# Optimization experiments

Hardware: AMD Instinct MI355X
Metric: run time of the kernel (lower is better)

## Reference

```python
import jax, jax.numpy as jnp
import numpy as np

B = 64; FEAT = 16; T = 32001; BANDS = 8; ND = 16
OUT_LEN = 32000; N_TAPS = 43; K_LATE = 1024
FLIP_PROB = 0.1  # 1 - stickiness (0.9)


def _dense(k, fan_in, fan_out, scale=1.0):
    return jax.random.normal(k, (fan_in, fan_out), jnp.float32) * (scale / np.sqrt(fan_in))


def setup_inputs() -> dict:
    key = jax.random.key(0)
    ks = jax.random.split(key, 20)
    z32 = lambda n: jnp.zeros((n,), jnp.float32)
    inp = {}
    inp['x'] = jax.random.normal(ks[0], (B, FEAT), jnp.float32)
    # stand-in LSTM decoder params: (B, FEAT) -> (B, T, BANDS)
    inp['lstm_W1'] = _dense(ks[1], FEAT, 64); inp['lstm_b1'] = z32(64)
    inp['lstm_W2'] = _dense(ks[2], 64, T * BANDS); inp['lstm_b2'] = z32(T * BANDS)
    # EDCToFDNMapper params
    inp['enc_W1'] = _dense(ks[3], 2 * BANDS, 64); inp['enc_b1'] = z32(64)
    inp['enc_W2'] = _dense(ks[4], 64, 64); inp['enc_b2'] = z32(64)
    inp['del_W1'] = _dense(ks[5], 3 + 64, 64); inp['del_b1'] = z32(64)
    inp['del_W2'] = _dense(ks[6], 64, ND); inp['del_b2'] = z32(ND)
    inp['alp_W1'] = _dense(ks[7], 64, 32); inp['alp_b1'] = z32(32)
    inp['alp_W2'] = _dense(ks[8], 32, ND); inp['alp_b2'] = z32(ND)
    inp['bet_W1'] = _dense(ks[9], 64, 32); inp['bet_b1'] = z32(32)
    inp['bet_W2'] = _dense(ks[10], 32, ND); inp['bet_b2'] = z32(ND)
    # EarlyReflections gains (nn.Parameter, zeros-init in torch; random here to exercise math)
    inp['early_gains'] = jax.random.normal(ks[11], (N_TAPS,), jnp.float32) * 0.1
    # DifferentiableFDN surrogate: causal decaying FIR reverb kernel
    decay = jnp.exp(-jnp.arange(K_LATE, dtype=jnp.float32) / 256.0)
    inp['late_kernel'] = jax.random.normal(ks[12], (K_LATE,), jnp.float32) * 0.05 * decay
    # sticky-sign flip events (constant random draws, flip prob = 1 - stickiness)
    inp['flips'] = (jax.random.uniform(ks[13], (B, OUT_LEN)) < FLIP_PROB).astype(jnp.int32)
    return inp


def _causal_conv(sig, gains):
    # torch: F.conv1d(x[:,None,:], gains.flip(0)[None,None,:], padding=K-1)[:, 0, :L]
    # (torch conv1d is correlation; flipping makes it true convolution with gains)
    K = gains.shape[0]
    y = jax.lax.conv_general_dilated(sig[:, None, :], gains[::-1][None, None, :], (1,),
                                     [(K - 1, K - 1)], dimension_numbers=('NCH', 'OIH', 'NCH'))
    return y[:, 0, :sig.shape[1]]


def _mlp2(h, W1, b1, W2, b2):  # Linear-ReLU-Linear
    return jax.nn.relu(h @ W1 + b1) @ W2 + b2


def reference(x, lstm_W1, lstm_b1, lstm_W2, lstm_b2,
              enc_W1, enc_b1, enc_W2, enc_b2,
              del_W1, del_b1, del_W2, del_b2,
              alp_W1, alp_b1, alp_W2, alp_b2,
              bet_W1, bet_b1, bet_W2, bet_b2,
              early_gains, late_kernel, flips):
    Bx = x.shape[0]
    # LSTM stand-in: (B, FEAT) -> (B, T, BANDS)
    edc_pred = _mlp2(x, lstm_W1, lstm_b1, lstm_W2, lstm_b2).reshape(Bx, T, BANDS)
    edc_1d = edc_pred.mean(axis=2)  # (B, T)
    # EDCToFDNMapper
    edc_mean = edc_pred.mean(axis=1)
    q1 = edc_pred[:, :T // 4, :].mean(axis=1)
    q4 = edc_pred[:, 3 * T // 4:, :].mean(axis=1)
    edc_feat = jnp.concatenate([edc_mean, q4 - q1], axis=1)  # (B, 2*BANDS)
    h = jax.nn.relu(_mlp2(edc_feat, enc_W1, enc_b1, enc_W2, enc_b2))  # Linear-ReLU-Linear-ReLU
    delay_in = jnp.concatenate([x[:, :3], h], axis=1)
    log_kappa = _mlp2(delay_in, del_W1, del_b1, del_W2, del_b2)
    alpha_raw = _mlp2(h, alp_W1, alp_b1, alp_W2, alp_b2)
    beta_raw = _mlp2(h, bet_W1, bet_b1, bet_W2, bet_b2)
    # late reverb (FDN surrogate) + early reflections, both causal convs on edc_1d
    late = _causal_conv(edc_1d, late_kernel)[:, :OUT_LEN]   # (B, 32000)
    early = _causal_conv(edc_1d, early_gains)[:, :OUT_LEN]  # (B, 32000)
    # sign-sticky phase reconstruction: signs = (-1)^cumsum(flips[:,1:]) (parallel parity scan)
    diff = edc_1d[:, :-1] - edc_1d[:, 1:]
    amp = jnp.sqrt(jnp.clip(diff, 0.0))  # (B, T-1) == (B, 32000)
    par = jnp.cumsum(flips.at[:, 0].set(0), axis=1) % 2  # loop starts at t=1; signs[:,0]=+1
    phase = amp * (1.0 - 2.0 * par.astype(amp.dtype))
    rir = (early + late) * phase
    return (rir, edc_pred, log_kappa, alpha_raw, beta_raw)
```

## Files before the change

kernel.cpp:

```cpp
#include <hip/hip_runtime.h>
#include <hip/hip_bf16.h>

#define LJ 256008
#define TN 32001
#define OUT_LEN 32000

typedef __attribute__((ext_vector_type(8))) short short8v;
typedef __attribute__((ext_vector_type(8))) __bf16 bf16x8;
typedef __attribute__((ext_vector_type(4))) float f32x4;

__device__ __forceinline__ unsigned short f2bu(float f) {
    union { __hip_bfloat16 h; unsigned short u; } cv; cv.h = __float2bfloat16(f); return cv.u;
}
__device__ __forceinline__ uint4 pack8(const unsigned short* h) {
    return make_uint4((unsigned)h[0] | ((unsigned)h[1] << 16),
                      (unsigned)h[2] | ((unsigned)h[3] << 16),
                      (unsigned)h[4] | ((unsigned)h[5] << 16),
                      (unsigned)h[6] | ((unsigned)h[7] << 16));
}
__device__ __forceinline__ f32x4 mfma16(uint4 a, uint4 b, f32x4 c) {
    union { uint4 u; short8v s; bf16x8 v; } ua, ub;
    ua.u = a; ub.u = b;
    return __builtin_amdgcn_mfma_f32_16x16x32_bf16(ua.v, ub.v, c, 0, 0, 0);
}

__global__ __launch_bounds__(256) void k_h1(const float* __restrict__ x,
                                            const float* __restrict__ W1,
                                            const float* __restrict__ b1,
                                            float* __restrict__ h1)
{
    int idx = blockIdx.x * 256 + threadIdx.x;
    if (idx >= 4096) return;
    int b = idx >> 6, i = idx & 63;
    float acc = b1[i];
    #pragma unroll
    for (int f = 0; f < 16; ++f)
        acc += x[b * 16 + f] * W1[f * 64 + i];
    h1[i * 64 + b] = fmaxf(acc, 0.f);
}

__global__ __launch_bounds__(512) void k_gemm(const float* __restrict__ W2,
                                              const float* __restrict__ b2,
                                              const float* __restrict__ h1,
                                              float* __restrict__ edc,
                                              float* __restrict__ edc1d,
                                              float* __restrict__ P)
{
    __shared__ float h1f[4096];
    __shared__ __align__(16) unsigned short afr[4096];
    __shared__ __align__(16) unsigned short bfr[8192];
    __shared__ float wband[2048];
    __shared__ float bband[32];
    int tid = threadIdx.x;
    long C0 = (long)blockIdx.x * 256;

    #pragma unroll
    for (int s = 0; s < 8; ++s) h1f[tid + 512 * s] = h1[tid + 512 * s];
    {
        int bt = tid >> 7, kb = (tid >> 6) & 1, l = tid & 63;
        int q = l >> 4, r = l & 15;
        unsigned short hh[8];
        #pragma unroll
        for (int e = 0; e < 8; ++e)
            hh[e] = f2bu(h1[(32 * kb + 8 * q + e) * 64 + 16 * bt + r]);
        *(uint4*)(&afr[tid * 8]) = pack8(hh);
    }
    #pragma unroll
    for (int s = 0; s < 4; ++s) {
        int en = tid + 512 * s;
        int i = en >> 5, tl = en & 31;
        long c8 = C0 + 8 * tl;
        float sum = 0.f;
        if (c8 + 7 < LJ) {
            float4 u0 = *(const float4*)(W2 + (long)i * LJ + c8);
            float4 u1 = *(const float4*)(W2 + (long)i * LJ + c8 + 4);
            sum = ((u0.x + u0.y) + (u0.z + u0.w)) + ((u1.x + u1.y) + (u1.z + u1.w));
        }
        wband[i * 32 + tl] = sum;
    }
    if (tid < 32) {
        long c8 = C0 + 8 * tid;
        float sum = 0.f;
        if (c8 + 7 < LJ) {
            float4 u0 = *(const float4*)(b2 + c8);
            float4 u1 = *(const float4*)(b2 + c8 + 4);
            sum = ((u0.x + u0.y) + (u0.z + u0.w)) + ((u1.x + u1.y) + (u1.z + u1.w));
        }
        bband[tid] = sum;
    }
    #pragma unroll
    for (int s = 0; s < 2; ++s) {
        int sl = tid + 512 * s;
        int ct = sl >> 6, l = sl & 63;
        int q = l >> 4, r = l & 15;
        long col = C0 + 16 * ct + r;
        unsigned short hh[8];
        #pragma unroll
        for (int e = 0; e < 8; ++e) {
            float v = (col < LJ) ? W2[(long)(8 * q + e) * LJ + col] : 0.f;
            hh[e] = f2bu(v);
        }
        *(uint4*)(&bfr[sl * 8]) = pack8(hh);
    }
    __syncthreads();

    int lane = tid & 63, wv = tid >> 6;
    int q = lane >> 4, r = lane & 15;
    f32x4 acc[2][4];
    #pragma unroll
    for (int c = 0; c < 2; ++c)
        #pragma unroll
        for (int b = 0; b < 4; ++b) acc[c][b] = (f32x4){0.f, 0.f, 0.f, 0.f};

    #pragma unroll
    for (int ctl = 0; ctl < 2; ++ctl) {
        int ct = wv * 2 + ctl;
        uint4 braw = *(const uint4*)(&bfr[(ct * 64 + lane) * 8]);
        #pragma unroll
        for (int bt = 0; bt < 4; ++bt) {
            uint4 araw = *(const uint4*)(&afr[((bt * 2 + 0) * 64 + lane) * 8]);
            acc[ctl][bt] = mfma16(araw, braw, acc[ctl][bt]);
        }
    }
    __syncthreads();
    #pragma unroll
    for (int s = 0; s < 2; ++s) {
        int sl = tid + 512 * s;
        int ct = sl >> 6, l = sl & 63;
        int qq = l >> 4, rr = l & 15;
        long col = C0 + 16 * ct + rr;
        unsigned short hh[8];
        #pragma unroll
        for (int e = 0; e < 8; ++e) {
            float v = (col < LJ) ? W2[(long)(32 + 8 * qq + e) * LJ + col] : 0.f;
            hh[e] = f2bu(v);
        }
        *(uint4*)(&bfr[sl * 8]) = pack8(hh);
    }
    __syncthreads();
    #pragma unroll
    for (int ctl = 0; ctl < 2; ++ctl) {
        int ct = wv * 2 + ctl;
        uint4 braw = *(const uint4*)(&bfr[(ct * 64 + lane) * 8]);
        #pragma unroll
        for (int bt = 0; bt < 4; ++bt) {
            uint4 araw = *(const uint4*)(&afr[((bt * 2 + 1) * 64 + lane) * 8]);
            acc[ctl][bt] = mfma16(araw, braw, acc[ctl][bt]);
        }
    }

    #pragma unroll
    for (int s = 0; s < 4; ++s) {
        int en = tid + 512 * s;
        int b = en >> 5, tl = en & 31;
        long c8 = C0 + 8 * tl;
        if (c8 + 7 < LJ) {
            float dot = bband[tl];
            #pragma unroll 8
            for (int i = 0; i < 64; ++i)
                dot += h1f[i * 64 + b] * wband[i * 32 + tl];
            edc1d[(long)b * TN + (C0 >> 3) + tl] = dot * 0.125f;
        }
    }

    float psum[4][4];
    #pragma unroll
    for (int bt = 0; bt < 4; ++bt)
        #pragma unroll
        for (int rg = 0; rg < 4; ++rg) psum[bt][rg] = 0.f;
    #pragma unroll
    for (int ctl = 0; ctl < 2; ++ctl) {
        int ct = wv * 2 + ctl;
        long col = C0 + 16 * ct + r;
        bool okc = col < LJ;
        float bias = okc ? b2[col] : 0.f;
        #pragma unroll
        for (int bt = 0; bt < 4; ++bt) {
            #pragma unroll
            for (int rg = 0; rg < 4; ++rg) {
                float v = acc[ctl][bt][rg] + bias;
                if (okc) edc[(long)(16 * bt + 4 * q + rg) * LJ + col] = v;
                float sps = v + __shfl_xor(v, 8);
                psum[bt][rg] += sps;
            }
        }
    }
    if (r < 8) {
        #pragma unroll
        for (int bt = 0; bt < 4; ++bt)
            #pragma unroll
            for (int rg = 0; rg < 4; ++rg)
                P[(long)blockIdx.x * 512 + (16 * bt + 4 * q + rg) * 8 + r] = psum[bt][rg];
    }
}

__global__ __launch_bounds__(512) void k_redsum(const float* __restrict__ P,
                                                float* __restrict__ sums)
{
    int g = blockIdx.x, t = threadIdx.x;
    int b = t >> 3, band = t & 7;
    int s0 = g * 16, s1 = s0 + 16;
    if (s1 > 1001) s1 = 1001;
    float all = 0.f, q1 = 0.f, q4 = 0.f;
    for (int blk = s0; blk < s1; ++blk) {
        float v = P[(long)blk * 512 + t];
        all += v;
        if (blk < 250) q1 += v;
        if (blk >= 750) q4 += v;
    }
    atomicAdd(&sums[b * 24 + band * 3 + 0], all);
    atomicAdd(&sums[b * 24 + band * 3 + 1], q1);
    atomicAdd(&sums[b * 24 + band * 3 + 2], q4);
}

__global__ __launch_bounds__(64) void k_mlp(const float* __restrict__ x,
    const float* __restrict__ sums,
    const float* __restrict__ eW1, const float* __restrict__ eb1,
    const float* __restrict__ eW2, const float* __restrict__ eb2,
    const float* __restrict__ dW1, const float* __restrict__ db1,
    const float* __restrict__ dW2, const float* __restrict__ db2,
    const float* __restrict__ aW1, const float* __restrict__ ab1,
    const float* __restrict__ aW2, const float* __restrict__ ab2,
    const float* __restrict__ bW1, const float* __restrict__ bb1,
    const float* __restrict__ bW2, const float* __restrict__ bb2,
    float* __restrict__ out_lk, float* __restrict__ out_a, float* __restrict__ out_b)
{
    int b = blockIdx.x, o = threadIdx.x;
    __shared__ float feat[16], a1[64], hh[64], t1[64];
    if (o < 16) {
        float v;
        if (o < 8) v = sums[b * 24 + o * 3] * (1.f / 32001.f);
        else {
            int band = o - 8;
            v = sums[b * 24 + band * 3 + 2] * (1.f / 8001.f)
              - sums[b * 24 + band * 3 + 1] * (1.f / 8000.f);
        }
        feat[o] = v;
    }
    __syncthreads();
    {   float acc = eb1[o];
        #pragma unroll
        for (int c = 0; c < 16; ++c) acc += feat[c] * eW1[c * 64 + o];
        a1[o] = fmaxf(acc, 0.f); }
    __syncthreads();
    {   float acc = eb2[o];
        for (int c = 0; c < 64; ++c) acc += a1[c] * eW2[c * 64 + o];
        hh[o] = fmaxf(acc, 0.f); }
    __syncthreads();
    {   float acc = db1[o];
        #pragma unroll
        for (int c = 0; c < 3; ++c) acc += x[b * 16 + c] * dW1[c * 64 + o];
        for (int c = 0; c < 64; ++c) acc += hh[c] * dW1[(3 + c) * 64 + o];
        t1[o] = fmaxf(acc, 0.f); }
    __syncthreads();
    if (o < 16) {
        float acc = db2[o];
        for (int c = 0; c < 64; ++c) acc += t1[c] * dW2[c * 16 + o];
        out_lk[b * 16 + o] = acc;
    }
    __syncthreads();
    if (o < 32) {
        float acc = ab1[o];
        for (int c = 0; c < 64; ++c) acc += hh[c] * aW1[c * 32 + o];
        t1[o] = fmaxf(acc, 0.f);
    }
    __syncthreads();
    if (o < 16) {
        float acc = ab2[o];
        for (int c = 0; c < 32; ++c) acc += t1[c] * aW2[c * 16 + o];
        out_a[b * 16 + o] = acc;
    }
    __syncthreads();
    if (o < 32) {
        float acc = bb1[o];
        for (int c = 0; c < 64; ++c) acc += hh[c] * bW1[c * 32 + o];
        t1[o] = fmaxf(acc, 0.f);
    }
    __syncthreads();
    if (o < 16) {
        float acc = bb2[o];
        for (int c = 0; c < 32; ++c) acc += t1[c] * bW2[c * 16 + o];
        out_b[b * 16 + o] = acc;
    }
}

__global__ __launch_bounds__(256) void k_par1(const int* __restrict__ flips,
                                              unsigned* __restrict__ parbits,
                                              unsigned* __restrict__ ctot)
{
    int b = blockIdx.x, c = blockIdx.y, tid = threadIdx.x;
    int t = c * 256 + tid;
    int bit = (t == 0) ? 0 : (flips[(long)b * OUT_LEN + t] & 1);
    int lane = tid & 63, wv = tid >> 6;
    unsigned long long mask = __ballot(bit != 0);
    int below = ((int)__popcll(mask & ((1ull << lane) - 1ull))) & 1;
    int incl = below ^ bit;
    __shared__ int wtot[4];
    if (lane == 0) wtot[wv] = ((int)__popcll(mask)) & 1;
    __syncthreads();
    int pre = 0;
    for (int w = 0; w < wv; ++w) pre ^= wtot[w];
    int inclB = pre ^ incl;
    unsigned long long m2 = __ballot(inclB != 0);
    if (lane == 0)  parbits[b * 1000 + c * 8 + wv * 2 + 0] = (unsigned)(m2 & 0xffffffffull);
    if (lane == 32) parbits[b * 1000 + c * 8 + wv * 2 + 1] = (unsigned)(m2 >> 32);
    if (tid == 0) ctot[c * 64 + b] = (unsigned)(wtot[0] ^ wtot[1] ^ wtot[2] ^ wtot[3]);
}

__global__ __launch_bounds__(64) void k_par2(const unsigned* __restrict__ ctot,
                                             unsigned* __restrict__ cpref)
{
    int b = threadIdx.x;
    unsigned carry = 0;
    for (int c = 0; c < 125; ++c) {
        cpref[c * 64 + b] = carry;
        carry ^= ctot[c * 64 + b];
    }
}

__global__ __launch_bounds__(512) void k_convm(const float* __restrict__ edc1d,
    const float* __restrict__ lk, const float* __restrict__ eg,
    const unsigned* __restrict__ parbits, const unsigned* __restrict__ cpref,
    float* __restrict__ rir)
{
    __shared__ float kerf[1024];
    __shared__ __align__(16) unsigned short afr[33 * 64 * 8];
    __shared__ __align__(16) unsigned short sbf[3136];
    __shared__ float sf32[2049];
    int b = blockIdx.x, tb0 = blockIdx.y * 2048, tid = threadIdx.x;
    const float* src = edc1d + (long)b * TN;
    for (int k = tid; k < 1024; k += 512)
        kerf[k] = lk[k] + (k < 43 ? eg[k] : 0.f);
    for (int ch = tid; ch < 388; ch += 512) {
        unsigned short h[8];
        #pragma unroll
        for (int e = 0; e < 8; ++e) {
            int gt = tb0 + ch * 8 + e - 1031;
            float v = (gt >= 0 && gt <= OUT_LEN) ? src[gt] : 0.f;
            h[e] = f2bu(v);
        }
        int cs = ch ^ ((ch >> 3) & 7);
        *(uint4*)(&sbf[cs * 8]) = pack8(h);
    }
    for (int u = tid; u < 2049; u += 512) {
        int gt = tb0 + u;
        sf32[u] = (gt <= OUT_LEN) ? src[gt] : 0.f;
    }
    __syncthreads();
    for (int sl = tid; sl < 33 * 64; sl += 512) {
        int kb = sl >> 6, l = sl & 63;
        int x0 = kb * 32 - 1 + (l & 15) - 8 * (l >> 4);
        unsigned short h[8];
        #pragma unroll
        for (int e = 0; e < 8; ++e) {
            int x = x0 - e;
            float v = (x >= 0 && x < 1024) ? kerf[x] : 0.f;
            h[e] = f2bu(v);
        }
        *(uint4*)(&afr[sl * 8]) = pack8(h);
    }
    __syncthreads();
    int lane = tid & 63, wv = tid >> 6;
    int tb = tb0 + wv * 256;
    int cq = wv * 256 + 16 * (lane & 15) + 8 * (lane >> 4) + 1032;
    f32x4 acc = {0.f, 0.f, 0.f, 0.f};
    for (int kb = 0; kb < 33; ++kb) {
        uint4 araw = *(const uint4*)(&afr[(kb * 64 + lane) * 8]);
        int ch = (cq - (kb << 5)) >> 3;
        int cs = ch ^ ((ch >> 3) & 7);
        uint4 braw = *(const uint4*)(&sbf[cs * 8]);
        acc = mfma16(araw, braw, acc);
    }
    int c = lane & 15, q = lane >> 4;
    int t4 = tb + 16 * c + 4 * q;
    if (t4 < OUT_LEN) {
        int u0 = t4 - tb0;
        unsigned pw = parbits[b * 1000 + (t4 >> 5)];
        unsigned cp = cpref[(t4 >> 8) * 64 + b] & 1u;
        int sh = t4 & 31;
        float sv[5];
        #pragma unroll
        for (int e = 0; e < 5; ++e) sv[e] = sf32[u0 + e];
        float r[4];
        #pragma unroll
        for (int reg = 0; reg < 4; ++reg) {
            float diff = sv[reg] - sv[reg + 1];
            float amp = diff > 0.f ? sqrtf(diff) : 0.f;
            unsigned p = ((pw >> (sh + reg)) & 1u) ^ cp;
            r[reg] = acc[reg] * amp * (p ? -1.f : 1.f);
        }
        *(float4*)(rir + (long)b * OUT_LEN + t4) = make_float4(r[0], r[1], r[2], r[3]);
    }
}

extern "C" void kernel_launch(void* const* d_in, const int* in_sizes, int n_in,
                              void* d_out, int out_size, void* d_ws, size_t ws_size,
                              hipStream_t stream) {
    (void)in_sizes; (void)n_in; (void)out_size; (void)ws_size;
    const float* x    = (const float*)d_in[0];
    const float* lW1  = (const float*)d_in[1];  const float* lb1 = (const float*)d_in[2];
    const float* lW2  = (const float*)d_in[3];  const float* lb2 = (const float*)d_in[4];
    const float* eW1  = (const float*)d_in[5];  const float* eb1 = (const float*)d_in[6];
    const float* eW2  = (const float*)d_in[7];  const float* eb2 = (const float*)d_in[8];
    const float* dW1  = (const float*)d_in[9];  const float* db1 = (const float*)d_in[10];
    const float* dW2  = (const float*)d_in[11]; const float* db2 = (const float*)d_in[12];
    const float* aW1  = (const float*)d_in[13]; const float* ab1 = (const float*)d_in[14];
    const float* aW2  = (const float*)d_in[15]; const float* ab2 = (const float*)d_in[16];
    const float* bW1  = (const float*)d_in[17]; const float* bb1 = (const float*)d_in[18];
    const float* bW2  = (const float*)d_in[19]; const float* bb2 = (const float*)d_in[20];
    const float* eg   = (const float*)d_in[21]; const float* lkk = (const float*)d_in[22];
    const int* flips  = (const int*)d_in[23];

    float* out = (float*)d_out;
    float* rir = out;
    float* edc = out + 2048000;
    float* olk = out + 18432512;
    float* oa  = out + 18433536;
    float* ob  = out + 18434560;

    char* wsb = (char*)d_ws;
    float*    ws_h1   = (float*)(wsb + 1024);
    unsigned* ws_ct   = (unsigned*)(wsb + 18432);
    unsigned* ws_cp   = (unsigned*)(wsb + 50688);
    unsigned* ws_pb   = (unsigned*)(wsb + 82944);
    float*    ws_sums = (float*)(wsb + 339200);
    float*    ws_e1d  = (float*)(wsb + 346112);
    float*    ws_part = (float*)(wsb + 8538368);

    hipMemsetAsync(ws_sums, 0, 64 * 24 * sizeof(float), stream);

    k_h1<<<16, 256, 0, stream>>>(x, lW1, lb1, ws_h1);
    k_par1<<<dim3(64, 125), 256, 0, stream>>>(flips, ws_pb, ws_ct);
    k_par2<<<1, 64, 0, stream>>>(ws_ct, ws_cp);
    k_gemm<<<1001, 512, 0, stream>>>(lW2, lb2, ws_h1, edc, ws_e1d, ws_part);
    k_redsum<<<63, 512, 0, stream>>>(ws_part, ws_sums);
    k_mlp<<<64, 64, 0, stream>>>(x, ws_sums, eW1, eb1, eW2, eb2, dW1, db1, dW2, db2,
                                 aW1, ab1, aW2, ab2, bW1, bb1, bW2, bb2, olk, oa, ob);
    k_convm<<<dim3(64, 16), 512, 0, stream>>>(ws_e1d, lkk, eg, ws_pb, ws_cp, rir);
}
```

Measured before the change: 116.0 us.

## Stage W2 tiles in LDS once via float4 loads, derive band sums and MFMA fragments

```diff
diff --git a/kernel.cpp b/kernel.cpp
--- a/kernel.cpp
+++ b/kernel.cpp
@@ -47,12 +47,13 @@
                                               float* __restrict__ P)
 {
     __shared__ float h1f[4096];
+    __shared__ float w2f[8192];
     __shared__ __align__(16) unsigned short afr[4096];
-    __shared__ __align__(16) unsigned short bfr[8192];
     __shared__ float wband[2048];
     __shared__ float bband[32];
     int tid = threadIdx.x;
     long C0 = (long)blockIdx.x * 256;
+    float4 z4 = make_float4(0.f, 0.f, 0.f, 0.f);
 
     #pragma unroll
     for (int s = 0; s < 8; ++s) h1f[tid + 512 * s] = h1[tid + 512 * s];
@@ -64,19 +65,6 @@
         for (int e = 0; e < 8; ++e)
             hh[e] = f2bu(h1[(32 * kb + 8 * q + e) * 64 + 16 * bt + r]);
         *(uint4*)(&afr[tid * 8]) = pack8(hh);
-    }
-    #pragma unroll
-    for (int s = 0; s < 4; ++s) {
-        int en = tid + 512 * s;
-        int i = en >> 5, tl = en & 31;
-        long c8 = C0 + 8 * tl;
-        float sum = 0.f;
-        if (c8 + 7 < LJ) {
-            float4 u0 = *(const float4*)(W2 + (long)i * LJ + c8);
-            float4 u1 = *(const float4*)(W2 + (long)i * LJ + c8 + 4);
-            sum = ((u0.x + u0.y) + (u0.z + u0.w)) + ((u1.x + u1.y) + (u1.z + u1.w));
-        }
-        wband[i * 32 + tl] = sum;
     }
     if (tid < 32) {
         long c8 = C0 + 8 * tid;
@@ -89,18 +77,12 @@
         bband[tid] = sum;
     }
     #pragma unroll
-    for (int s = 0; s < 2; ++s) {
-        int sl = tid + 512 * s;
-        int ct = sl >> 6, l = sl & 63;
-        int q = l >> 4, r = l & 15;
-        long col = C0 + 16 * ct + r;
-        unsigned short hh[8];
-        #pragma unroll
-        for (int e = 0; e < 8; ++e) {
-            float v = (col < LJ) ? W2[(long)(8 * q + e) * LJ + col] : 0.f;
-            hh[e] = f2bu(v);
-        }
-        *(uint4*)(&bfr[sl * 8]) = pack8(hh);
+    for (int s = 0; s < 4; ++s) {
+        int slot = tid + 512 * s;
+        int row = slot >> 6, c4 = slot & 63;
+        long col = C0 + 4 * c4;
+        float4 v = (col < LJ) ? *(const float4*)(W2 + (long)row * LJ + col) : z4;
+        *(float4*)(&w2f[row * 256 + 4 * c4]) = v;
     }
     __syncthreads();
 
@@ -113,9 +95,20 @@
         for (int b = 0; b < 4; ++b) acc[c][b] = (f32x4){0.f, 0.f, 0.f, 0.f};
 
     #pragma unroll
+    for (int s = 0; s < 2; ++s) {
+        int en = tid + 512 * s;
+        int i = en >> 5, tl = en & 31;
+        const float* p = &w2f[i * 256 + 8 * tl];
+        wband[i * 32 + tl] = ((p[0] + p[1]) + (p[2] + p[3])) + ((p[4] + p[5]) + (p[6] + p[7]));
+    }
+    #pragma unroll
     for (int ctl = 0; ctl < 2; ++ctl) {
         int ct = wv * 2 + ctl;
-        uint4 braw = *(const uint4*)(&bfr[(ct * 64 + lane) * 8]);
+        unsigned short hh[8];
+        #pragma unroll
+        for (int e = 0; e < 8; ++e)
+            hh[e] = f2bu(w2f[(8 * q + e) * 256 + 16 * ct + r]);
+        uint4 braw = pack8(hh);
         #pragma unroll
         for (int bt = 0; bt < 4; ++bt) {
             uint4 araw = *(const uint4*)(&afr[((bt * 2 + 0) * 64 + lane) * 8]);
@@ -124,30 +117,36 @@
     }
     __syncthreads();
     #pragma unroll
+    for (int s = 0; s < 4; ++s) {
+        int slot = tid + 512 * s;
+        int row = slot >> 6, c4 = slot & 63;
+        long col = C0 + 4 * c4;
+        float4 v = (col < LJ) ? *(const float4*)(W2 + (long)(32 + row) * LJ + col) : z4;
+        *(float4*)(&w2f[row * 256 + 4 * c4]) = v;
+    }
+    __syncthreads();
+    #pragma unroll
     for (int s = 0; s < 2; ++s) {
-        int sl = tid + 512 * s;
-        int ct = sl >> 6, l = sl & 63;
-        int qq = l >> 4, rr = l & 15;
-        long col = C0 + 16 * ct + rr;
-        unsigned short hh[8];
-        #pragma unroll
-        for (int e = 0; e < 8; ++e) {
-            float v = (col < LJ) ? W2[(long)(32 + 8 * qq + e) * LJ + col] : 0.f;
-            hh[e] = f2bu(v);
-        }
-        *(uint4*)(&bfr[sl * 8]) = pack8(hh);
-    }
-    __syncthreads();
+        int en = tid + 512 * s;
+        int i2 = en >> 5, tl = en & 31;
+        const float* p = &w2f[i2 * 256 + 8 * tl];
+        wband[(32 + i2) * 32 + tl] = ((p[0] + p[1]) + (p[2] + p[3])) + ((p[4] + p[5]) + (p[6] + p[7]));
+    }
     #pragma unroll
     for (int ctl = 0; ctl < 2; ++ctl) {
         int ct = wv * 2 + ctl;
-        uint4 braw = *(const uint4*)(&bfr[(ct * 64 + lane) * 8]);
+        unsigned short hh[8];
+        #pragma unroll
+        for (int e = 0; e < 8; ++e)
+            hh[e] = f2bu(w2f[(8 * q + e) * 256 + 16 * ct + r]);
+        uint4 braw = pack8(hh);
         #pragma unroll
         for (int bt = 0; bt < 4; ++bt) {
             uint4 araw = *(const uint4*)(&afr[((bt * 2 + 1) * 64 + lane) * 8]);
             acc[ctl][bt] = mfma16(araw, braw, acc[ctl][bt]);
         }
     }
+    __syncthreads();
 
     #pragma unroll
     for (int s = 0; s < 4; ++s) {
```

Measured after the change: 101.3 us. -12.7%, faster.
